# Performance work log

Measured on AMD Instinct MI355X. Metric: run time of the kernel, lower is better.

Reference implementation:

```python
import jax, jax.numpy as jnp
import numpy as np

N = 50000
E = 800000
EPS = 1e-5
GAT_SLOPE = 0.2   # PyG GATConv internal LeakyReLU slope
ACT_SLOPE = 0.01  # decoder's LeakyReLU(alpha)


def setup_inputs() -> dict:
    key = jax.random.key(0)
    ks = jax.random.split(key, 10)
    d = {
        "embeddings": jax.random.normal(ks[0], (N, 64), jnp.float32),
        "edge_index": jax.random.randint(ks[1], (2, E), 0, N, jnp.int64),
        "W1": jax.random.normal(ks[2], (64, 128), jnp.float32) * 0.1,
        "a_src1": jax.random.normal(ks[3], (128,), jnp.float32) * 0.1,
        "a_dst1": jax.random.normal(ks[4], (128,), jnp.float32) * 0.1,
        "b1": jnp.zeros((128,), jnp.float32),
        "gamma1": jnp.ones((128,), jnp.float32),
        "beta1": jnp.zeros((128,), jnp.float32),
        "W2": jax.random.normal(ks[5], (128, 256), jnp.float32) * 0.1,
        "a_src2": jax.random.normal(ks[6], (256,), jnp.float32) * 0.1,
        "a_dst2": jax.random.normal(ks[7], (256,), jnp.float32) * 0.1,
        "b2": jnp.zeros((256,), jnp.float32),
        "gamma2": jnp.ones((256,), jnp.float32),
        "beta2": jnp.zeros((256,), jnp.float32),
        "Wf": jax.random.normal(ks[8], (256, 256), jnp.float32) * 0.1,
        "bf": jnp.zeros((256,), jnp.float32),
    }
    return d


def gat_conv(x, src, dst, W, a_s, a_d, b):
    # PyG GATConv, heads=1, concat=False, add_self_loops=True (loops appended in caller)
    h = x @ W                                    # [N, out]
    e = h @ a_s                                  # alpha_src per node
    f = h @ a_d                                  # alpha_dst per node
    logits = jax.nn.leaky_relu(e[src] + f[dst], GAT_SLOPE)   # [E']
    # scatter-softmax over destination neighborhoods
    m = jax.ops.segment_max(logits, dst, num_segments=N)
    ex = jnp.exp(logits - m[dst])
    denom = jax.ops.segment_sum(ex, dst, num_segments=N)
    alpha = ex / denom[dst]                      # [E']
    out = jax.ops.segment_sum(h[src] * alpha[:, None], dst, num_segments=N)
    return out + b


def batch_norm(x, gamma, beta):
    mu = jnp.mean(x, axis=0)
    var = jnp.mean((x - mu) ** 2, axis=0)        # biased, as torch BN uses
    return (x - mu) * jax.lax.rsqrt(var + EPS) * gamma + beta


def reference(embeddings, edge_index, W1, a_src1, a_dst1, b1, gamma1, beta1,
              W2, a_src2, a_dst2, b2, gamma2, beta2, Wf, bf):
    loops = jnp.arange(N, dtype=edge_index.dtype)
    src = jnp.concatenate([edge_index[0], loops])
    dst = jnp.concatenate([edge_index[1], loops])
    x = embeddings
    for (W, a_s, a_d, b, g, be) in [
        (W1, a_src1, a_dst1, b1, gamma1, beta1),
        (W2, a_src2, a_dst2, b2, gamma2, beta2),
    ]:
        x = gat_conv(x, src, dst, W, a_s, a_d, b)
        x = batch_norm(x, g, be)
        x = jax.nn.leaky_relu(x, ACT_SLOPE)
        # dropout: identity (eval mode)
    return x @ Wf + bf
```

## Files before the change

### kernel.cpp

```cpp
#include <hip/hip_runtime.h>
#include <hip/hip_fp16.h>
#include <math.h>

#define N_NODES 50000
#define N_EDGES 800000
#define N_TOT   850000
#define EPS_BN  1e-5f
#define GAT_SLOPE 0.2f
#define ACT_SLOPE 0.01f
#define NBUCK   ((N_NODES + 255) / 256)
#define BCAP    5120
#define K1_CH   4096
#define K1_NB   ((N_TOT + K1_CH - 1) / K1_CH)
#define GB64    ((N_NODES + 63) / 64)
#define NREP    8

typedef _Float16 half8_t __attribute__((ext_vector_type(8)));
typedef _Float16 half4_t __attribute__((ext_vector_type(4)));
typedef _Float16 half2_t __attribute__((ext_vector_type(2)));
typedef float    f32x4   __attribute__((ext_vector_type(4)));

__device__ __forceinline__ float wred_max(float x) {
#pragma unroll
    for (int m = 32; m; m >>= 1) x = fmaxf(x, __shfl_xor(x, m, 64));
    return x;
}
__device__ __forceinline__ float wred_sum(float x) {
#pragma unroll
    for (int m = 32; m; m >>= 1) x += __shfl_xor(x, m, 64);
    return x;
}
__device__ __forceinline__ int wred_sum_i(int x) {
#pragma unroll
    for (int m = 32; m; m >>= 1) x += __shfl_xor(x, m, 64);
    return x;
}

__device__ __forceinline__ void wf_perm(const float* __restrict__ W,
                                        _Float16* __restrict__ wt,
                                        int K, int C, int i) {
    int j   = i & 7;
    int l   = (i >> 3) & 63;
    int rest = i >> 9;
    int tt  = rest & 3;
    int ksf = rest >> 2;
    int KS  = K >> 5;
    int cb  = ksf / KS, ks = ksf - cb * KS;
    int k   = ks * 32 + (l >> 4) * 8 + j;
    int c   = cb * 64 + tt * 16 + (l & 15);
    wt[i] = (_Float16)W[k * C + c];
}

__global__ void init_misc(const float* __restrict__ W1, const float* __restrict__ W2,
                          const float* __restrict__ Wf, _Float16* __restrict__ wt1,
                          _Float16* __restrict__ wt2, _Float16* __restrict__ wtf,
                          int* __restrict__ bcnt,
                          float2* __restrict__ gsum1, float2* __restrict__ gsum2,
                          const float* __restrict__ as1, const float* __restrict__ ad1,
                          const float* __restrict__ as2, const float* __restrict__ ad2,
                          float* __restrict__ va1, float* __restrict__ vb1,
                          float* __restrict__ va2, float* __restrict__ vb2) {
    int i = blockIdx.x * 256 + threadIdx.x;
    if (i < NBUCK) bcnt[i] = 0;
    if (i < NREP * 128) gsum1[i] = make_float2(0.f, 0.f);
    if (i < NREP * 256) gsum2[i] = make_float2(0.f, 0.f);
    if (i < 8192) {
        wf_perm(W1, wt1, 64, 128, i);
    } else if (i < 8192 + 32768) {
        wf_perm(W2, wt2, 128, 256, i - 8192);
    } else if (i < 8192 + 32768 + 65536) {
        wf_perm(Wf, wtf, 256, 256, i - 40960);
    } else if (i < 106496 + 384) {
        int j = i - 106496;
        if (j < 64) {
            float s = 0.f;
            for (int c = 0; c < 128; ++c) s += W1[j * 128 + c] * as1[c];
            va1[j] = s;
        } else if (j < 128) {
            int k = j - 64; float s = 0.f;
            for (int c = 0; c < 128; ++c) s += W1[k * 128 + c] * ad1[c];
            vb1[k] = s;
        } else if (j < 256) {
            int k = j - 128; float s = 0.f;
            for (int c = 0; c < 256; ++c) s += W2[k * 256 + c] * as2[c];
            va2[k] = s;
        } else {
            int k = j - 256; float s = 0.f;
            for (int c = 0; c < 256; ++c) s += W2[k * 256 + c] * ad2[c];
            vb2[k] = s;
        }
    }
}

__global__ __launch_bounds__(256) void
append_emb(const int* __restrict__ ei, int* __restrict__ bcnt,
           unsigned* __restrict__ bedge,
           const float* __restrict__ emb, const float* __restrict__ va,
           const float* __restrict__ vb, _Float16* __restrict__ embh,
           float* __restrict__ e_n, float* __restrict__ f_n) {
    const int t = threadIdx.x;
    if ((int)blockIdx.x < K1_NB) {
        __shared__ int lcnt[NBUCK], lrank[NBUCK], gbase[NBUCK];
        const int base = blockIdx.x * K1_CH;
        const int nE = min(K1_CH, N_TOT - base);
        for (int i = t; i < NBUCK; i += 256) { lcnt[i] = 0; lrank[i] = 0; }
        __syncthreads();
        unsigned r[16];
#pragma unroll
        for (int j = 0; j < 16; ++j) {
            int i = t + j * 256;
            if (i < nE) {
                int e = base + i;
                int s, d;
                if (e < N_EDGES) { s = ei[e]; d = ei[N_EDGES + e]; }
                else { s = e - N_EDGES; d = s; }
                r[j] = ((unsigned)d << 16) | (unsigned)s;
                atomicAdd(&lcnt[d >> 8], 1);
            }
        }
        __syncthreads();
        if (t < NBUCK && lcnt[t] > 0) gbase[t] = atomicAdd(&bcnt[t], lcnt[t]);
        __syncthreads();
#pragma unroll
        for (int j = 0; j < 16; ++j) {
            int i = t + j * 256;
            if (i < nE) {
                unsigned v = r[j];
                int bk = v >> 24;
                int gp = gbase[bk] + atomicAdd(&lrank[bk], 1);
                if (gp < BCAP) bedge[(size_t)bk * BCAP + gp] = v;
            }
        }
        return;
    }
    int rr = ((int)blockIdx.x - K1_NB) * 4 + (t >> 6);
    if (rr >= N_NODES) return;
    int l = t & 63;
    float v = emb[(size_t)rr * 64 + l];
    embh[(size_t)rr * 64 + l] = (_Float16)v;
    float pe = wred_sum(v * va[l]);
    float pf = wred_sum(v * vb[l]);
    if (l == 0) { e_n[rr] = pe; f_n[rr] = pf; }
}

__global__ __launch_bounds__(256) void
bucket_csr(const int* __restrict__ bcnt, const unsigned* __restrict__ bedge,
           int* __restrict__ ptr, int* __restrict__ srcs) {
    __shared__ int lcnt[256], lptr[256], lrank[256];
    __shared__ int wsum[4];
    __shared__ int sbase;
    const int b = blockIdx.x, t = threadIdx.x;
    lcnt[t] = 0; lrank[t] = 0;
    if (t < 64) {
        int s = 0;
        for (int j = t; j < b; j += 64) s += bcnt[j];
        s = wred_sum_i(s);
        if (t == 0) sbase = s;
    }
    __syncthreads();
    const int cnt = min(bcnt[b], BCAP);
    const int base0 = sbase;
    const unsigned* eb = bedge + (size_t)b * BCAP;
    for (int i = t; i < cnt; i += 256) atomicAdd(&lcnt[(eb[i] >> 16) & 255], 1);
    __syncthreads();
    int lane = t & 63, w = t >> 6;
    int v = lcnt[t];
    int x = v;
#pragma unroll
    for (int off = 1; off < 64; off <<= 1) {
        int y = __shfl_up(x, off, 64);
        if (lane >= off) x += y;
    }
    if (lane == 63) wsum[w] = x;
    __syncthreads();
    if (t == 0) {
        int s = 0;
#pragma unroll
        for (int i = 0; i < 4; ++i) { int tmp = wsum[i]; wsum[i] = s; s += tmp; }
    }
    __syncthreads();
    lptr[t] = x - v + wsum[w];
    __syncthreads();
    int d = b * 256 + t;
    if (d < N_NODES) ptr[d] = base0 + lptr[t];
    if (b == NBUCK - 1 && t == 0) ptr[N_NODES] = base0 + cnt;
    for (int i = t; i < cnt; i += 256) {
        unsigned v2 = eb[i];
        int dl = (v2 >> 16) & 255;
        int pos = base0 + lptr[dl] + atomicAdd(&lrank[dl], 1);
        srcs[pos] = (int)(v2 & 0xFFFFu);
    }
}

__global__ __launch_bounds__(256) void
ef_dots(const _Float16* __restrict__ x, const float2* __restrict__ gsum,
        const float* __restrict__ gamma, const float* __restrict__ beta,
        const float* __restrict__ va, const float* __restrict__ vb,
        _Float16* __restrict__ z, float* __restrict__ e_n,
        float* __restrict__ f_n) {
    int r = blockIdx.x * 4 + (threadIdx.x >> 6);
    if (r >= N_NODES) return;
    int l = threadIdx.x & 63;
    int c = 2 * l;
    float4 sq = make_float4(0.f, 0.f, 0.f, 0.f);
#pragma unroll
    for (int rep = 0; rep < NREP; ++rep) {
        float4 p = *(const float4*)&gsum[rep * 128 + c];
        sq.x += p.x; sq.y += p.y; sq.z += p.z; sq.w += p.w;
    }
    float mu0 = sq.x / N_NODES, mu1 = sq.z / N_NODES;
    float sc0 = gamma[c]     * rsqrtf(sq.y / N_NODES - mu0 * mu0 + EPS_BN);
    float sc1 = gamma[c + 1] * rsqrtf(sq.w / N_NODES - mu1 * mu1 + EPS_BN);
    float sh0 = beta[c]     - mu0 * sc0;
    float sh1 = beta[c + 1] - mu1 * sc1;
    half2_t hv = *(const half2_t*)&x[(size_t)r * 128 + c];
    float x0 = (float)hv[0] * sc0 + sh0;
    float x1 = (float)hv[1] * sc1 + sh1;
    x0 = x0 > 0.f ? x0 : ACT_SLOPE * x0;
    x1 = x1 > 0.f ? x1 : ACT_SLOPE * x1;
    half2_t zo = { (_Float16)x0, (_Float16)x1 };
    *(half2_t*)&z[(size_t)r * 128 + c] = zo;
    float pe = wred_sum(x0 * va[c] + x1 * va[c + 1]);
    float pf = wred_sum(x0 * vb[c] + x1 * vb[c + 1]);
    if (l == 0) { e_n[r] = pe; f_n[r] = pf; }
}

template<int K, int C, int CB, typename OutT, bool STATS, bool BNIN>
__global__ __launch_bounds__(256) void
gemm_mfma(const _Float16* __restrict__ x, const _Float16* __restrict__ wt,
          const float* __restrict__ bias, OutT* __restrict__ out, int n,
          float2* __restrict__ gsum_out, const float2* __restrict__ gsum_in,
          const float* __restrict__ gamma, const float* __restrict__ beta) {
    constexpr int NW_C = CB / 64;
    constexpr int RT   = NW_C;
    constexpr int NCB  = C / CB;
    constexpr int KS   = K / 32;
    constexpr int LK   = K + 8;
    constexpr int LCB  = CB + 4;
    constexpr size_t SMB = ((size_t)64 * LK * 2 > (size_t)64 * LCB * 4)
                             ? (size_t)64 * LK * 2 : (size_t)64 * LCB * 4;
    __shared__ alignas(16) char smem[SMB];
    _Float16* xs  = (_Float16*)smem;
    float*   cbuf = (float*)smem;
    __shared__ float cs_sh[STATS ? CB : 1];
    __shared__ float cq_sh[STATS ? CB : 1];
    __shared__ float sc_in[BNIN ? K : 1];
    __shared__ float sh_in[BNIN ? K : 1];

    const int rb = blockIdx.x / NCB;
    const int cblk = blockIdx.x - rb * NCB;
    const int row0 = rb * 64;
    const int colB = cblk * CB;
    const int t = threadIdx.x;

    if (STATS) {
        for (int c = t; c < CB; c += 256) { cs_sh[c] = 0.f; cq_sh[c] = 0.f; }
    }
    if constexpr (BNIN) {
        for (int c = t; c < K; c += 256) {
            float s = 0.f, q = 0.f;
#pragma unroll
            for (int rep = 0; rep < NREP; ++rep) {
                float2 p = gsum_in[rep * K + c];
                s += p.x; q += p.y;
            }
            float mu = s / N_NODES;
            float sc = gamma[c] * rsqrtf(q / N_NODES - mu * mu + EPS_BN);
            sc_in[c] = sc;
            sh_in[c] = beta[c] - mu * sc;
        }
        __syncthreads();
    }

    for (int i = t * 8; i < 64 * K; i += 256 * 8) {
        int r = i / K, c = i - (i / K) * K;
        half8_t v = {};
        if (row0 + r < n) v = *(const half8_t*)&x[(size_t)(row0 + r) * K + c];
        if constexpr (BNIN) {
#pragma unroll
            for (int j = 0; j < 8; ++j) {
                float f = (float)v[j] * sc_in[c + j] + sh_in[c + j];
                v[j] = (_Float16)(f > 0.f ? f : ACT_SLOPE * f);
            }
        }
        *(half8_t*)&xs[r * LK + c] = v;
    }
    __syncthreads();

    const int w = t >> 6, l = t & 63;
    const int l16 = l & 15, quad = l >> 4;
    const int lc0 = (w % NW_C) * 64;
    const int gc0 = colB + lc0;
    const int mbase = (w / NW_C) * (16 * NW_C);
    const _Float16* wtw = wt + (size_t)(gc0 >> 6) * KS * 4 * 512 + l * 8;

    f32x4 acc[RT][4] = {};
    half8_t bA[4], bB[4];
    auto loadB = [&](int k0, half8_t* bf) {
        const _Float16* p = wtw + (size_t)(k0 >> 5) * 4 * 512;
#pragma unroll
        for (int tt = 0; tt < 4; ++tt)
            bf[tt] = *(const half8_t*)&p[tt * 512];
    };
    auto doMM = [&](int k0, half8_t* bf) {
        half8_t a[RT];
#pragma unroll
        for (int rt = 0; rt < RT; ++rt)
            a[rt] = *(const half8_t*)&xs[(mbase + rt * 16 + l16) * LK + k0 + quad * 8];
#pragma unroll
        for (int rt = 0; rt < RT; ++rt)
#pragma unroll
            for (int tt = 0; tt < 4; ++tt)
                acc[rt][tt] = __builtin_amdgcn_mfma_f32_16x16x32_f16(a[rt], bf[tt],
                                                                     acc[rt][tt], 0, 0, 0);
    };
    loadB(0, bA);
#pragma unroll
    for (int k0 = 0; k0 < K; k0 += 64) {
        loadB(k0 + 32, bB);
        doMM(k0, bA);
        if (k0 + 64 < K) loadB(k0 + 64, bA);
        doMM(k0 + 32, bB);
    }

    __syncthreads();
#pragma unroll
    for (int rt = 0; rt < RT; ++rt) {
#pragma unroll
        for (int tt = 0; tt < 4; ++tt) {
            int lcol = lc0 + tt * 16 + l16;
            float bb = bias ? bias[colB + lcol] : 0.f;
            float s = 0.f, q = 0.f;
#pragma unroll
            for (int i = 0; i < 4; ++i) {
                int lrow = mbase + rt * 16 + quad * 4 + i;
                float v = acc[rt][tt][i] + bb;
                cbuf[lrow * LCB + lcol] = v;
                if (STATS && row0 + lrow < n) { s += v; q += v * v; }
            }
            if constexpr (STATS) {
                s += __shfl_xor(s, 16, 64); s += __shfl_xor(s, 32, 64);
                q += __shfl_xor(q, 16, 64); q += __shfl_xor(q, 32, 64);
                if (quad == 0) {
                    atomicAdd(&cs_sh[lcol], s);
                    atomicAdd(&cq_sh[lcol], q);
                }
            }
        }
    }
    __syncthreads();
    if constexpr (STATS) {
        float2* gdst = gsum_out + (size_t)(rb & (NREP - 1)) * C + colB;
        for (int c = t; c < CB; c += 256) {
            atomicAdd(&gdst[c].x, cs_sh[c]);
            atomicAdd(&gdst[c].y, cq_sh[c]);
        }
    }
    for (int i = t * 4; i < 64 * CB; i += 256 * 4) {
        int r = i / CB, c = i - (i / CB) * CB;
        if (row0 + r < n) {
            float4 v4 = *(const float4*)&cbuf[r * LCB + c];
            if constexpr (__is_same(OutT, float)) {
                *(float4*)&out[(size_t)(row0 + r) * C + colB + c] = v4;
            } else {
                half4_t h4 = { (_Float16)v4.x, (_Float16)v4.y,
                               (_Float16)v4.z, (_Float16)v4.w };
                *(half4_t*)&out[(size_t)(row0 + r) * C + colB + c] = h4;
            }
        }
    }
}

template<int C>
__global__ __launch_bounds__(256) void
attn_aggregate(const _Float16* __restrict__ h, const int* __restrict__ srcs,
               const int* __restrict__ ptr, const float* __restrict__ e_n,
               const float* __restrict__ f_n, _Float16* __restrict__ out) {
    constexpr int RL = C / 8;
    constexpr int G  = 64 / RL;
    int d = blockIdx.x * 4 + (threadIdx.x >> 6);
    if (d >= N_NODES) return;
    int l  = threadIdx.x & 63;
    int b0 = ptr[d], b1 = ptr[d + 1];
    int deg = b1 - b0;
    float fd = f_n[d];
    const int g  = l / RL;
    const int cl = l % RL;
    float acc[8] = {0.f, 0.f, 0.f, 0.f, 0.f, 0.f, 0.f, 0.f};

    if (deg <= 64) {
        int sj = 0; float lg = -1e30f;
        if (l < deg) {
            sj = srcs[b0 + l];
            float v = e_n[sj] + fd;
            lg = v > 0.f ? v : GAT_SLOPE * v;
        }
        float m  = wred_max(lg);
        float e0 = (l < deg) ? __expf(lg - m) : 0.f;
        float ex = e0 / wred_sum(e0);

        int jj = 0;
        for (; jj + 4 * G <= deg; jj += 4 * G) {
            float wk[4]; int sk[4];
#pragma unroll
            for (int k = 0; k < 4; ++k) {
                int j = jj + k * G + g;
                wk[k] = __shfl(ex, j, 64);
                sk[k] = __shfl(sj, j, 64);
            }
            half8_t v[4];
#pragma unroll
            for (int k = 0; k < 4; ++k)
                v[k] = *(const half8_t*)&h[(size_t)sk[k] * C + cl * 8];
#pragma unroll
            for (int k = 0; k < 4; ++k)
#pragma unroll
                for (int i = 0; i < 8; ++i)
                    acc[i] += wk[k] * (float)v[k][i];
        }
        for (; jj + 2 * G <= deg; jj += 2 * G) {
            float w1 = __shfl(ex, jj + g, 64);
            int   s1 = __shfl(sj, jj + g, 64);
            float w2 = __shfl(ex, jj + G + g, 64);
            int   s2 = __shfl(sj, jj + G + g, 64);
            half8_t v1 = *(const half8_t*)&h[(size_t)s1 * C + cl * 8];
            half8_t v2 = *(const half8_t*)&h[(size_t)s2 * C + cl * 8];
#pragma unroll
            for (int i = 0; i < 8; ++i)
                acc[i] += w1 * (float)v1[i] + w2 * (float)v2[i];
        }
        for (; jj < deg; jj += G) {
            int j = jj + g;
            float wk = __shfl(ex, j, 64);
            int   sk = __shfl(sj, j, 64);
            if (j < deg) {
                half8_t v = *(const half8_t*)&h[(size_t)sk * C + cl * 8];
#pragma unroll
                for (int i = 0; i < 8; ++i) acc[i] += wk * (float)v[i];
            }
        }
    } else {
        float m_l = -1e30f, den_l = 0.f;
        for (int j = b0 + l; j < b1; j += 64) {
            float lg = e_n[srcs[j]] + fd;
            lg = lg > 0.f ? lg : GAT_SLOPE * lg;
            float nm = fmaxf(m_l, lg);
            den_l = den_l * __expf(m_l - nm) + __expf(lg - nm);
            m_l = nm;
        }
        float m = wred_max(m_l);
        float inv = 1.f / wred_sum(den_l * __expf(m_l - m));
        for (int c0 = b0; c0 < b1; c0 += 64) {
            int jl = c0 + l;
            int sj = 0; float ex = 0.f;
            if (jl < b1) {
                sj = srcs[jl];
                float lg = e_n[sj] + fd;
                lg = lg > 0.f ? lg : GAT_SLOPE * lg;
                ex = __expf(lg - m) * inv;
            }
            int nE = min(64, b1 - c0);
            for (int jj = 0; jj < nE; jj += 2 * G) {
                int j1 = jj + g, j2 = jj + G + g;
                float w1 = __shfl(ex, j1, 64);
                int   s1 = __shfl(sj, j1, 64);
                float w2 = __shfl(ex, j2, 64);
                int   s2 = __shfl(sj, j2, 64);
                half8_t v1 = *(const half8_t*)&h[(size_t)s1 * C + cl * 8];
                half8_t v2 = *(const half8_t*)&h[(size_t)s2 * C + cl * 8];
#pragma unroll
                for (int i = 0; i < 8; ++i)
                    acc[i] += w1 * (float)v1[i] + w2 * (float)v2[i];
            }
        }
    }
#pragma unroll
    for (int mm = RL; mm < 64; mm <<= 1)
#pragma unroll
        for (int i = 0; i < 8; ++i) acc[i] += __shfl_xor(acc[i], mm, 64);
    if (g == 0) {
        int c = cl * 8;
        half8_t o;
#pragma unroll
        for (int i = 0; i < 8; ++i) o[i] = (_Float16)acc[i];
        *(half8_t*)&out[(size_t)d * C + c] = o;
    }
}

extern "C" void kernel_launch(void* const* d_in, const int* in_sizes, int n_in,
                              void* d_out, int out_size, void* d_ws, size_t ws_size,
                              hipStream_t stream) {
    const float* emb  = (const float*)d_in[0];
    const int*   ei   = (const int*)  d_in[1];
    const float* W1   = (const float*)d_in[2];
    const float* as1  = (const float*)d_in[3];
    const float* ad1  = (const float*)d_in[4];
    const float* b1   = (const float*)d_in[5];
    const float* g1   = (const float*)d_in[6];
    const float* be1  = (const float*)d_in[7];
    const float* W2   = (const float*)d_in[8];
    const float* as2  = (const float*)d_in[9];
    const float* ad2  = (const float*)d_in[10];
    const float* b2   = (const float*)d_in[11];
    const float* g2   = (const float*)d_in[12];
    const float* be2  = (const float*)d_in[13];
    const float* Wf   = (const float*)d_in[14];
    const float* bf   = (const float*)d_in[15];
    float* out = (float*)d_out;

    char* w = (char*)d_ws;
    auto alloc = [&](size_t bytes) {
        char* p = w;
        w += (bytes + 255) & ~(size_t)255;
        return (void*)p;
    };
    _Float16* embh = (_Float16*)alloc((size_t)N_NODES * 64 * 2);
    _Float16* agg1 = (_Float16*)alloc((size_t)N_NODES * 64 * 2);
    _Float16* out1 = (_Float16*)alloc((size_t)N_NODES * 128 * 2);
    _Float16* agg2 = (_Float16*)alloc((size_t)N_NODES * 128 * 2);
    _Float16* out2 = (_Float16*)alloc((size_t)N_NODES * 256 * 2);
    _Float16* z1h  = embh;
    unsigned* bedge = (unsigned*)out2;
    float*  e_n  = (float*) alloc((size_t)N_NODES * 4);
    float*  f_n  = (float*) alloc((size_t)N_NODES * 4);
    int*    srcs = (int*)   alloc((size_t)N_TOT * 4);
    int*    bcnt = (int*)   alloc((size_t)NBUCK * 4);
    int*    ptr  = (int*)   alloc((size_t)(N_NODES + 1) * 4);
    float2* gsum1 = (float2*)alloc((size_t)NREP * 128 * 8);
    float2* gsum2 = (float2*)alloc((size_t)NREP * 256 * 8);
    float*  va1  = (float*) alloc(64 * 4);
    float*  vb1  = (float*) alloc(64 * 4);
    float*  va2  = (float*) alloc(128 * 4);
    float*  vb2  = (float*) alloc(128 * 4);
    _Float16* wt1 = (_Float16*)alloc((size_t)64 * 128 * 2);
    _Float16* wt2 = (_Float16*)alloc((size_t)128 * 256 * 2);
    _Float16* wtf = (_Float16*)alloc((size_t)256 * 256 * 2);

    const int RW4 = (N_NODES + 3) / 4;

    init_misc<<<(106496 + 384 + 255) / 256, 256, 0, stream>>>(
        W1, W2, Wf, wt1, wt2, wtf, bcnt, gsum1, gsum2,
        as1, ad1, as2, ad2, va1, vb1, va2, vb2);

    append_emb<<<K1_NB + RW4, 256, 0, stream>>>(
        ei, bcnt, bedge, emb, va1, vb1, embh, e_n, f_n);

    bucket_csr<<<NBUCK, 256, 0, stream>>>(bcnt, bedge, ptr, srcs);

    attn_aggregate<64><<<RW4, 256, 0, stream>>>(embh, srcs, ptr, e_n, f_n, agg1);

    gemm_mfma<64, 128, 128, _Float16, true, false><<<GB64, 256, 0, stream>>>(
        agg1, wt1, b1, out1, N_NODES, gsum1, nullptr, nullptr, nullptr);

    ef_dots<<<RW4, 256, 0, stream>>>(out1, gsum1, g1, be1, va2, vb2, z1h, e_n, f_n);

    attn_aggregate<128><<<RW4, 256, 0, stream>>>(z1h, srcs, ptr, e_n, f_n, agg2);

    gemm_mfma<128, 256, 128, _Float16, true, false><<<GB64 * 2, 256, 0, stream>>>(
        agg2, wt2, b2, out2, N_NODES, gsum2, nullptr, nullptr, nullptr);

    gemm_mfma<256, 256, 128, float, false, true><<<GB64 * 2, 256, 0, stream>>>(
        out2, wtf, bf, out, N_NODES, nullptr, gsum2, g2, be2);
}
```

Before: 282.0 us.

## Fuse attention aggregation into the following MFMA GEMM per 64-row tile

Attention-weighted neighbor aggregation now runs inside the GEMM kernel. Each block aggregates 64 destination rows straight into shared memory and then multiplies them by the weight matrix with MFMA. This removes the agg1/agg2 intermediate global round trips and two kernel launches. In exchange, each block now does the irregular gather serially over 16 rows per wave before any MFMA work, and the layer-2 kernel runs one block per 64 rows covering all 256 columns instead of two column blocks. That halves the block count and may reduce latency hiding. Buffer aliasing is also changed so that z1h and bedge get their own allocations.

```diff
diff --git a/kernel.cpp b/kernel.cpp
--- a/kernel.cpp
+++ b/kernel.cpp
@@ -225,12 +225,233 @@
     if (l == 0) { e_n[r] = pe; f_n[r] = pf; }
 }
 
-template<int K, int C, int CB, typename OutT, bool STATS, bool BNIN>
+template<int K>
+__device__ __forceinline__ void
+aggregate_dst(const _Float16* __restrict__ h, const int* __restrict__ srcs,
+              const int* __restrict__ ptr, const float* __restrict__ e_n,
+              const float* __restrict__ f_n, int d, int l,
+              _Float16* __restrict__ xrow) {
+    constexpr int RL = K / 8;
+    constexpr int G  = 64 / RL;
+    int b0 = ptr[d], b1 = ptr[d + 1];
+    int deg = b1 - b0;
+    float fd = f_n[d];
+    const int g  = l / RL;
+    const int cl = l % RL;
+    float acc[8] = {0.f, 0.f, 0.f, 0.f, 0.f, 0.f, 0.f, 0.f};
+
+    if (deg <= 64) {
+        int sj = 0; float lg = -1e30f;
+        if (l < deg) {
+            sj = srcs[b0 + l];
+            float v = e_n[sj] + fd;
+            lg = v > 0.f ? v : GAT_SLOPE * v;
+        }
+        float m  = wred_max(lg);
+        float e0 = (l < deg) ? __expf(lg - m) : 0.f;
+        float ex = e0 / wred_sum(e0);
+
+        int jj = 0;
+        for (; jj + 4 * G <= deg; jj += 4 * G) {
+            float wk[4]; int sk[4];
+#pragma unroll
+            for (int k = 0; k < 4; ++k) {
+                int j = jj + k * G + g;
+                wk[k] = __shfl(ex, j, 64);
+                sk[k] = __shfl(sj, j, 64);
+            }
+            half8_t v[4];
+#pragma unroll
+            for (int k = 0; k < 4; ++k)
+                v[k] = *(const half8_t*)&h[(size_t)sk[k] * K + cl * 8];
+#pragma unroll
+            for (int k = 0; k < 4; ++k)
+#pragma unroll
+                for (int i = 0; i < 8; ++i)
+                    acc[i] += wk[k] * (float)v[k][i];
+        }
+        for (; jj + 2 * G <= deg; jj += 2 * G) {
+            float w1 = __shfl(ex, jj + g, 64);
+            int   s1 = __shfl(sj, jj + g, 64);
+            float w2 = __shfl(ex, jj + G + g, 64);
+            int   s2 = __shfl(sj, jj + G + g, 64);
+            half8_t v1 = *(const half8_t*)&h[(size_t)s1 * K + cl * 8];
+            half8_t v2 = *(const half8_t*)&h[(size_t)s2 * K + cl * 8];
+#pragma unroll
+            for (int i = 0; i < 8; ++i)
+                acc[i] += w1 * (float)v1[i] + w2 * (float)v2[i];
+        }
+        for (; jj < deg; jj += G) {
+            int j = jj + g;
+            float wk = __shfl(ex, j, 64);
+            int   sk = __shfl(sj, j, 64);
+            if (j < deg) {
+                half8_t v = *(const half8_t*)&h[(size_t)sk * K + cl * 8];
+#pragma unroll
+                for (int i = 0; i < 8; ++i) acc[i] += wk * (float)v[i];
+            }
+        }
+    } else {
+        float m_l = -1e30f, den_l = 0.f;
+        for (int j = b0 + l; j < b1; j += 64) {
+            float lg = e_n[srcs[j]] + fd;
+            lg = lg > 0.f ? lg : GAT_SLOPE * lg;
+            float nm = fmaxf(m_l, lg);
+            den_l = den_l * __expf(m_l - nm) + __expf(lg - nm);
+            m_l = nm;
+        }
+        float m = wred_max(m_l);
+        float inv = 1.f / wred_sum(den_l * __expf(m_l - m));
+        for (int c0 = b0; c0 < b1; c0 += 64) {
+            int jl = c0 + l;
+            int sj = 0; float ex = 0.f;
+            if (jl < b1) {
+                sj = srcs[jl];
+                float lg = e_n[sj] + fd;
+                lg = lg > 0.f ? lg : GAT_SLOPE * lg;
+                ex = __expf(lg - m) * inv;
+            }
+            int nE = min(64, b1 - c0);
+            for (int jj = 0; jj < nE; jj += 2 * G) {
+                int j1 = jj + g, j2 = jj + G + g;
+                float w1 = __shfl(ex, j1, 64);
+                int   s1 = __shfl(sj, j1, 64);
+                float w2 = __shfl(ex, j2, 64);
+                int   s2 = __shfl(sj, j2, 64);
+                half8_t v1 = *(const half8_t*)&h[(size_t)s1 * K + cl * 8];
+                half8_t v2 = *(const half8_t*)&h[(size_t)s2 * K + cl * 8];
+#pragma unroll
+                for (int i = 0; i < 8; ++i)
+                    acc[i] += w1 * (float)v1[i] + w2 * (float)v2[i];
+            }
+        }
+    }
+#pragma unroll
+    for (int mm = RL; mm < 64; mm <<= 1)
+#pragma unroll
+        for (int i = 0; i < 8; ++i) acc[i] += __shfl_xor(acc[i], mm, 64);
+    if (g == 0) {
+        half8_t o;
+#pragma unroll
+        for (int i = 0; i < 8; ++i) o[i] = (_Float16)acc[i];
+        *(half8_t*)&xrow[cl * 8] = o;
+    }
+}
+
+template<int K, int C>
 __global__ __launch_bounds__(256) void
-gemm_mfma(const _Float16* __restrict__ x, const _Float16* __restrict__ wt,
-          const float* __restrict__ bias, OutT* __restrict__ out, int n,
-          float2* __restrict__ gsum_out, const float2* __restrict__ gsum_in,
-          const float* __restrict__ gamma, const float* __restrict__ beta) {
+attn_gemm(const _Float16* __restrict__ h, const int* __restrict__ srcs,
+          const int* __restrict__ ptr, const float* __restrict__ e_n,
+          const float* __restrict__ f_n, const _Float16* __restrict__ wt,
+          const float* __restrict__ bias, _Float16* __restrict__ out, int n,
+          float2* __restrict__ gsum_out) {
+    constexpr int NW_C = C / 64;
+    constexpr int RT   = NW_C;
+    constexpr int KS   = K / 32;
+    constexpr int LK   = K + 8;
+    constexpr int LC   = C + 8;
+    constexpr size_t SMB = ((size_t)(64 * LK) > (size_t)(64 * LC)
+                              ? (size_t)(64 * LK) : (size_t)(64 * LC)) * 2;
+    __shared__ alignas(16) char smem[SMB];
+    _Float16* xs = (_Float16*)smem;
+    _Float16* cb = (_Float16*)smem;
+    __shared__ float cs_sh[C], cq_sh[C];
+
+    const int rb = blockIdx.x;
+    const int row0 = rb * 64;
+    const int t = threadIdx.x;
+    const int w = t >> 6, l = t & 63;
+
+    for (int c = t; c < C; c += 256) { cs_sh[c] = 0.f; cq_sh[c] = 0.f; }
+
+    for (int it = 0; it < 16; ++it) {
+        int dl = w * 16 + it;
+        int d  = row0 + dl;
+        if (d < n) {
+            aggregate_dst<K>(h, srcs, ptr, e_n, f_n, d, l, &xs[dl * LK]);
+        } else if (l < K / 8) {
+            *(half8_t*)&xs[dl * LK + l * 8] = half8_t{};
+        }
+    }
+    __syncthreads();
+
+    const int l16 = l & 15, quad = l >> 4;
+    const int lc0 = (w % NW_C) * 64;
+    const int mbase = (w / NW_C) * (16 * NW_C);
+    const _Float16* wtw = wt + (size_t)(lc0 >> 6) * KS * 4 * 512 + l * 8;
+
+    f32x4 acc[RT][4] = {};
+    half8_t bA[4], bB[4];
+    auto loadB = [&](int k0, half8_t* bf) {
+        const _Float16* p = wtw + (size_t)(k0 >> 5) * 4 * 512;
+#pragma unroll
+        for (int tt = 0; tt < 4; ++tt)
+            bf[tt] = *(const half8_t*)&p[tt * 512];
+    };
+    auto doMM = [&](int k0, half8_t* bf) {
+        half8_t a[RT];
+#pragma unroll
+        for (int rt = 0; rt < RT; ++rt)
+            a[rt] = *(const half8_t*)&xs[(mbase + rt * 16 + l16) * LK + k0 + quad * 8];
+#pragma unroll
+        for (int rt = 0; rt < RT; ++rt)
+#pragma unroll
+            for (int tt = 0; tt < 4; ++tt)
+                acc[rt][tt] = __builtin_amdgcn_mfma_f32_16x16x32_f16(a[rt], bf[tt],
+                                                                     acc[rt][tt], 0, 0, 0);
+    };
+    loadB(0, bA);
+#pragma unroll
+    for (int k0 = 0; k0 < K; k0 += 64) {
+        loadB(k0 + 32, bB);
+        doMM(k0, bA);
+        if (k0 + 64 < K) loadB(k0 + 64, bA);
+        doMM(k0 + 32, bB);
+    }
+
+    __syncthreads();
+#pragma unroll
+    for (int rt = 0; rt < RT; ++rt) {
+#pragma unroll
+        for (int tt = 0; tt < 4; ++tt) {
+            int lcol = lc0 + tt * 16 + l16;
+            float bb = bias[lcol];
+            float s = 0.f, q = 0.f;
+#pragma unroll
+            for (int i = 0; i < 4; ++i) {
+                int lrow = mbase + rt * 16 + quad * 4 + i;
+                float v = acc[rt][tt][i] + bb;
+                cb[lrow * LC + lcol] = (_Float16)v;
+                if (row0 + lrow < n) { s += v; q += v * v; }
+            }
+            s += __shfl_xor(s, 16, 64); s += __shfl_xor(s, 32, 64);
+            q += __shfl_xor(q, 16, 64); q += __shfl_xor(q, 32, 64);
+            if (quad == 0) {
+                atomicAdd(&cs_sh[lcol], s);
+                atomicAdd(&cq_sh[lcol], q);
+            }
+        }
+    }
+    __syncthreads();
+    float2* gdst = gsum_out + (size_t)(rb & (NREP - 1)) * C;
+    for (int c = t; c < C; c += 256) {
+        atomicAdd(&gdst[c].x, cs_sh[c]);
+        atomicAdd(&gdst[c].y, cq_sh[c]);
+    }
+    for (int i = t * 8; i < 64 * C; i += 256 * 8) {
+        int r = i / C, c = i - (i / C) * C;
+        if (row0 + r < n)
+            *(half8_t*)&out[(size_t)(row0 + r) * C + c] =
+                *(const half8_t*)&cb[r * LC + c];
+    }
+}
+
+template<int K, int C, int CB>
+__global__ __launch_bounds__(256) void
+gemm_final(const _Float16* __restrict__ x, const _Float16* __restrict__ wt,
+           const float* __restrict__ bias, float* __restrict__ out, int n,
+           const float2* __restrict__ gsum_in, const float* __restrict__ gamma,
+           const float* __restrict__ beta) {
     constexpr int NW_C = CB / 64;
     constexpr int RT   = NW_C;
     constexpr int NCB  = C / CB;
@@ -242,10 +463,8 @@
     __shared__ alignas(16) char smem[SMB];
     _Float16* xs  = (_Float16*)smem;
     float*   cbuf = (float*)smem;
-    __shared__ float cs_sh[STATS ? CB : 1];
-    __shared__ float cq_sh[STATS ? CB : 1];
-    __shared__ float sc_in[BNIN ? K : 1];
-    __shared__ float sh_in[BNIN ? K : 1];
+    __shared__ float sc_in[K];
+    __shared__ float sh_in[K];
 
     const int rb = blockIdx.x / NCB;
     const int cblk = blockIdx.x - rb * NCB;
@@ -253,35 +472,28 @@
     const int colB = cblk * CB;
     const int t = threadIdx.x;
 
-    if (STATS) {
-        for (int c = t; c < CB; c += 256) { cs_sh[c] = 0.f; cq_sh[c] = 0.f; }
-    }
-    if constexpr (BNIN) {
-        for (int c = t; c < K; c += 256) {
-            float s = 0.f, q = 0.f;
-#pragma unroll
-            for (int rep = 0; rep < NREP; ++rep) {
-                float2 p = gsum_in[rep * K + c];
-                s += p.x; q += p.y;
-            }
-            float mu = s / N_NODES;
-            float sc = gamma[c] * rsqrtf(q / N_NODES - mu * mu + EPS_BN);
-            sc_in[c] = sc;
-            sh_in[c] = beta[c] - mu * sc;
-        }
-        __syncthreads();
-    }
+    for (int c = t; c < K; c += 256) {
+        float s = 0.f, q = 0.f;
+#pragma unroll
+        for (int rep = 0; rep < NREP; ++rep) {
+            float2 p = gsum_in[rep * K + c];
+            s += p.x; q += p.y;
+        }
+        float mu = s / N_NODES;
+        float sc = gamma[c] * rsqrtf(q / N_NODES - mu * mu + EPS_BN);
+        sc_in[c] = sc;
+        sh_in[c] = beta[c] - mu * sc;
+    }
+    __syncthreads();
 
     for (int i = t * 8; i < 64 * K; i += 256 * 8) {
         int r = i / K, c = i - (i / K) * K;
         half8_t v = {};
         if (row0 + r < n) v = *(const half8_t*)&x[(size_t)(row0 + r) * K + c];
-        if constexpr (BNIN) {
-#pragma unroll
-            for (int j = 0; j < 8; ++j) {
-                float f = (float)v[j] * sc_in[c + j] + sh_in[c + j];
-                v[j] = (_Float16)(f > 0.f ? f : ACT_SLOPE * f);
-            }
+#pragma unroll
+        for (int j = 0; j < 8; ++j) {
+            float f = (float)v[j] * sc_in[c + j] + sh_in[c + j];
+            v[j] = (_Float16)(f > 0.f ? f : ACT_SLOPE * f);
         }
         *(half8_t*)&xs[r * LK + c] = v;
     }
@@ -329,161 +541,20 @@
 #pragma unroll
         for (int tt = 0; tt < 4; ++tt) {
             int lcol = lc0 + tt * 16 + l16;
-            float bb = bias ? bias[colB + lcol] : 0.f;
-            float s = 0.f, q = 0.f;
+            float bb = bias[colB + lcol];
 #pragma unroll
             for (int i = 0; i < 4; ++i) {
                 int lrow = mbase + rt * 16 + quad * 4 + i;
-                float v = acc[rt][tt][i] + bb;
-                cbuf[lrow * LCB + lcol] = v;
-                if (STATS && row0 + lrow < n) { s += v; q += v * v; }
-            }
-            if constexpr (STATS) {
-                s += __shfl_xor(s, 16, 64); s += __shfl_xor(s, 32, 64);
-                q += __shfl_xor(q, 16, 64); q += __shfl_xor(q, 32, 64);
-                if (quad == 0) {
-                    atomicAdd(&cs_sh[lcol], s);
-                    atomicAdd(&cq_sh[lcol], q);
-                }
-            }
-        }
-    }
-    __syncthreads();
-    if constexpr (STATS) {
-        float2* gdst = gsum_out + (size_t)(rb & (NREP - 1)) * C + colB;
-        for (int c = t; c < CB; c += 256) {
-            atomicAdd(&gdst[c].x, cs_sh[c]);
-            atomicAdd(&gdst[c].y, cq_sh[c]);
-        }
-    }
+                cbuf[lrow * LCB + lcol] = acc[rt][tt][i] + bb;
+            }
+        }
+    }
+    __syncthreads();
     for (int i = t * 4; i < 64 * CB; i += 256 * 4) {
         int r = i / CB, c = i - (i / CB) * CB;
-        if (row0 + r < n) {
-            float4 v4 = *(const float4*)&cbuf[r * LCB + c];
-            if constexpr (__is_same(OutT, float)) {
-                *(float4*)&out[(size_t)(row0 + r) * C + colB + c] = v4;
-            } else {
-                half4_t h4 = { (_Float16)v4.x, (_Float16)v4.y,
-                               (_Float16)v4.z, (_Float16)v4.w };
-                *(half4_t*)&out[(size_t)(row0 + r) * C + colB + c] = h4;
-            }
-        }
-    }
-}
-
-template<int C>
-__global__ __launch_bounds__(256) void
-attn_aggregate(const _Float16* __restrict__ h, const int* __restrict__ srcs,
-               const int* __restrict__ ptr, const float* __restrict__ e_n,
-               const float* __restrict__ f_n, _Float16* __restrict__ out) {
-    constexpr int RL = C / 8;
-    constexpr int G  = 64 / RL;
-    int d = blockIdx.x * 4 + (threadIdx.x >> 6);
-    if (d >= N_NODES) return;
-    int l  = threadIdx.x & 63;
-    int b0 = ptr[d], b1 = ptr[d + 1];
-    int deg = b1 - b0;
-    float fd = f_n[d];
-    const int g  = l / RL;
-    const int cl = l % RL;
-    float acc[8] = {0.f, 0.f, 0.f, 0.f, 0.f, 0.f, 0.f, 0.f};
-
-    if (deg <= 64) {
-        int sj = 0; float lg = -1e30f;
-        if (l < deg) {
-            sj = srcs[b0 + l];
-            float v = e_n[sj] + fd;
-            lg = v > 0.f ? v : GAT_SLOPE * v;
-        }
-        float m  = wred_max(lg);
-        float e0 = (l < deg) ? __expf(lg - m) : 0.f;
-        float ex = e0 / wred_sum(e0);
-
-        int jj = 0;
-        for (; jj + 4 * G <= deg; jj += 4 * G) {
-            float wk[4]; int sk[4];
-#pragma unroll
-            for (int k = 0; k < 4; ++k) {
-                int j = jj + k * G + g;
-                wk[k] = __shfl(ex, j, 64);
-                sk[k] = __shfl(sj, j, 64);
-            }
-            half8_t v[4];
-#pragma unroll
-            for (int k = 0; k < 4; ++k)
-                v[k] = *(const half8_t*)&h[(size_t)sk[k] * C + cl * 8];
-#pragma unroll
-            for (int k = 0; k < 4; ++k)
-#pragma unroll
-                for (int i = 0; i < 8; ++i)
-                    acc[i] += wk[k] * (float)v[k][i];
-        }
-        for (; jj + 2 * G <= deg; jj += 2 * G) {
-            float w1 = __shfl(ex, jj + g, 64);
-            int   s1 = __shfl(sj, jj + g, 64);
-            float w2 = __shfl(ex, jj + G + g, 64);
-            int   s2 = __shfl(sj, jj + G + g, 64);
-            half8_t v1 = *(const half8_t*)&h[(size_t)s1 * C + cl * 8];
-            half8_t v2 = *(const half8_t*)&h[(size_t)s2 * C + cl * 8];
-#pragma unroll
-            for (int i = 0; i < 8; ++i)
-                acc[i] += w1 * (float)v1[i] + w2 * (float)v2[i];
-        }
-        for (; jj < deg; jj += G) {
-            int j = jj + g;
-            float wk = __shfl(ex, j, 64);
-            int   sk = __shfl(sj, j, 64);
-            if (j < deg) {
-                half8_t v = *(const half8_t*)&h[(size_t)sk * C + cl * 8];
-#pragma unroll
-                for (int i = 0; i < 8; ++i) acc[i] += wk * (float)v[i];
-            }
-        }
-    } else {
-        float m_l = -1e30f, den_l = 0.f;
-        for (int j = b0 + l; j < b1; j += 64) {
-            float lg = e_n[srcs[j]] + fd;
-            lg = lg > 0.f ? lg : GAT_SLOPE * lg;
-            float nm = fmaxf(m_l, lg);
-            den_l = den_l * __expf(m_l - nm) + __expf(lg - nm);
-            m_l = nm;
-        }
-        float m = wred_max(m_l);
-        float inv = 1.f / wred_sum(den_l * __expf(m_l - m));
-        for (int c0 = b0; c0 < b1; c0 += 64) {
-            int jl = c0 + l;
-            int sj = 0; float ex = 0.f;
-            if (jl < b1) {
-                sj = srcs[jl];
-                float lg = e_n[sj] + fd;
-                lg = lg > 0.f ? lg : GAT_SLOPE * lg;
-                ex = __expf(lg - m) * inv;
-            }
-            int nE = min(64, b1 - c0);
-            for (int jj = 0; jj < nE; jj += 2 * G) {
-                int j1 = jj + g, j2 = jj + G + g;
-                float w1 = __shfl(ex, j1, 64);
-                int   s1 = __shfl(sj, j1, 64);
-                float w2 = __shfl(ex, j2, 64);
-                int   s2 = __shfl(sj, j2, 64);
-                half8_t v1 = *(const half8_t*)&h[(size_t)s1 * C + cl * 8];
-                half8_t v2 = *(const half8_t*)&h[(size_t)s2 * C + cl * 8];
-#pragma unroll
-                for (int i = 0; i < 8; ++i)
-                    acc[i] += w1 * (float)v1[i] + w2 * (float)v2[i];
-            }
-        }
-    }
-#pragma unroll
-    for (int mm = RL; mm < 64; mm <<= 1)
-#pragma unroll
-        for (int i = 0; i < 8; ++i) acc[i] += __shfl_xor(acc[i], mm, 64);
-    if (g == 0) {
-        int c = cl * 8;
-        half8_t o;
-#pragma unroll
-        for (int i = 0; i < 8; ++i) o[i] = (_Float16)acc[i];
-        *(half8_t*)&out[(size_t)d * C + c] = o;
+        if (row0 + r < n)
+            *(float4*)&out[(size_t)(row0 + r) * C + colB + c] =
+                *(const float4*)&cbuf[r * LCB + c];
     }
 }
 
@@ -515,12 +586,10 @@
         return (void*)p;
     };
     _Float16* embh = (_Float16*)alloc((size_t)N_NODES * 64 * 2);
-    _Float16* agg1 = (_Float16*)alloc((size_t)N_NODES * 64 * 2);
     _Float16* out1 = (_Float16*)alloc((size_t)N_NODES * 128 * 2);
-    _Float16* agg2 = (_Float16*)alloc((size_t)N_NODES * 128 * 2);
+    _Float16* z1h  = (_Float16*)alloc((size_t)N_NODES * 128 * 2);
     _Float16* out2 = (_Float16*)alloc((size_t)N_NODES * 256 * 2);
-    _Float16* z1h  = embh;
-    unsigned* bedge = (unsigned*)out2;
+    unsigned* bedge = (unsigned*)alloc((size_t)NBUCK * BCAP * 4);
     float*  e_n  = (float*) alloc((size_t)N_NODES * 4);
     float*  f_n  = (float*) alloc((size_t)N_NODES * 4);
     int*    srcs = (int*)   alloc((size_t)N_TOT * 4);
@@ -547,18 +616,14 @@
 
     bucket_csr<<<NBUCK, 256, 0, stream>>>(bcnt, bedge, ptr, srcs);
 
-    attn_aggregate<64><<<RW4, 256, 0, stream>>>(embh, srcs, ptr, e_n, f_n, agg1);
-
-    gemm_mfma<64, 128, 128, _Float16, true, false><<<GB64, 256, 0, stream>>>(
-        agg1, wt1, b1, out1, N_NODES, gsum1, nullptr, nullptr, nullptr);
+    attn_gemm<64, 128><<<GB64, 256, 0, stream>>>(
+        embh, srcs, ptr, e_n, f_n, wt1, b1, out1, N_NODES, gsum1);
 
     ef_dots<<<RW4, 256, 0, stream>>>(out1, gsum1, g1, be1, va2, vb2, z1h, e_n, f_n);
 
-    attn_aggregate<128><<<RW4, 256, 0, stream>>>(z1h, srcs, ptr, e_n, f_n, agg2);
-
-    gemm_mfma<128, 256, 128, _Float16, true, false><<<GB64 * 2, 256, 0, stream>>>(
-        agg2, wt2, b2, out2, N_NODES, gsum2, nullptr, nullptr, nullptr);
-
-    gemm_mfma<256, 256, 128, float, false, true><<<GB64 * 2, 256, 0, stream>>>(
-        out2, wtf, bf, out, N_NODES, nullptr, gsum2, g2, be2);
-}
+    attn_gemm<128, 256><<<GB64, 256, 0, stream>>>(
+        z1h, srcs, ptr, e_n, f_n, wt2, b2, out2, N_NODES, gsum2);
+
+    gemm_final<256, 256, 128><<<GB64 * 2, 256, 0, stream>>>(
+        out2, wtf, bf, out, N_NODES, gsum2, g2, be2);
+}
```

Measured after the change: 361.5 us. 1.28x slower.
